# Kernel optimization log

Measured on AMD Instinct MI355X. Metric: run time of the kernel, lower is better.

The kernel has to match this reference:

```python
import jax, jax.numpy as jnp
import numpy as np

# Dimensions (TinyLlama-like)
B, T = 4, 1024
D = 2048          # hidden_size
H, DH = 32, 64    # heads, head_dim
HK = 8            # kv heads (GQA, n_rep = 4)
RQ, RKV = 32, 32  # per-head SVD ranks
RO, RF = 1024, 1024
I = 5632          # intermediate_size
THETA = 10000.0
EPS = 1e-5


def setup_inputs() -> dict:
    key = jax.random.key(0)
    ks = jax.random.split(key, 16)
    p = lambda k, s: jax.random.normal(k, s, jnp.float32) * 0.02
    return {
        "x": jax.random.normal(ks[0], (B, T, D), jnp.float32),
        "ln1_w": jnp.ones((D,), jnp.float32),
        "ln2_w": jnp.ones((D,), jnp.float32),
        "q_Us": p(ks[1], (H, DH, RQ)),  "q_V": p(ks[2], (H, RQ, D)),
        "k_Us": p(ks[3], (HK, DH, RKV)), "k_V": p(ks[4], (HK, RKV, D)),
        "v_Us": p(ks[5], (HK, DH, RKV)), "v_V": p(ks[6], (HK, RKV, D)),
        "o_Us": p(ks[7], (D, RO)),  "o_V": p(ks[8], (RO, H * DH)),
        "g_Us": p(ks[9], (I, RF)),  "g_V": p(ks[10], (RF, D)),
        "u_Us": p(ks[11], (I, RF)), "u_V": p(ks[12], (RF, D)),
        "d_Us": p(ks[13], (D, RF)), "d_V": p(ks[14], (RF, I)),
    }


def _rms(x, w):
    return x * jax.lax.rsqrt(jnp.mean(x * x, axis=-1, keepdims=True) + EPS) * w


def _rope_cos_sin(t_len, dh, dtype):
    half = dh // 2
    inv_freq = 1.0 / (THETA ** (jnp.arange(half, dtype=jnp.float32) / half))
    ang = jnp.arange(t_len, dtype=jnp.float32)[:, None] * inv_freq[None, :]  # [T, half]
    return jnp.cos(ang).astype(dtype), jnp.sin(ang).astype(dtype)


def _apply_rope(x, cos, sin):
    # x: [B,h,T,Dh], LLaMA half-split rotation
    half = x.shape[-1] // 2
    x1, x2 = x[..., :half], x[..., half:]
    c = cos[None, None]  # [1,1,T,half]
    s = sin[None, None]
    return jnp.concatenate([x1 * c - x2 * s, x2 * c + x1 * s], axis=-1)


def reference(x, ln1_w, ln2_w, q_Us, q_V, k_Us, k_V, v_Us, v_V,
              o_Us, o_V, g_Us, g_V, u_Us, u_V, d_Us, d_V):
    b, t, d = x.shape
    h1 = _rms(x, ln1_w)

    # per-head low-rank projections: y_h = x @ V_h^T @ Us_h^T
    q = jnp.einsum('bhtr,hdr->bhtd', jnp.einsum('btD,hrD->bhtr', h1, q_V), q_Us)  # [B,H,T,Dh]
    k = jnp.einsum('bhtr,hdr->bhtd', jnp.einsum('btD,hrD->bhtr', h1, k_V), k_Us)  # [B,Hk,T,Dh]
    v = jnp.einsum('bhtr,hdr->bhtd', jnp.einsum('btD,hrD->bhtr', h1, v_V), v_Us)

    cos, sin = _rope_cos_sin(t, DH, x.dtype)
    q = _apply_rope(q, cos, sin)
    k = _apply_rope(k, cos, sin)

    n_rep = H // HK
    k = jnp.repeat(k, n_rep, axis=1)  # _repeat_kv
    v = jnp.repeat(v, n_rep, axis=1)

    scale = 1.0 / np.sqrt(DH)
    scores = jnp.einsum('bhtd,bhsd->bhts', q, k) * scale
    causal = jnp.tril(jnp.ones((t, t), bool))
    scores = jnp.where(causal[None, None], scores, jnp.finfo(scores.dtype).min)
    attn = jax.nn.softmax(scores, axis=-1)
    ctx = jnp.einsum('bhts,bhsd->bhtd', attn, v)
    ctx = ctx.transpose(0, 2, 1, 3).reshape(b, t, H * DH)

    # low-rank output proj: o = ctx @ o_V^T @ o_Us^T
    attn_out = jnp.einsum('btr,Dr->btD', jnp.einsum('btk,rk->btr', ctx, o_V), o_Us)
    x = x + attn_out

    # SwiGLU MLP with low-rank factors
    h2 = _rms(x, ln2_w)
    g = jnp.einsum('btr,ir->bti', jnp.einsum('btD,rD->btr', h2, g_V), g_Us)
    u = jnp.einsum('btr,ir->bti', jnp.einsum('btD,rD->btr', h2, u_V), u_Us)
    ff = jax.nn.silu(g) * u
    down = jnp.einsum('btr,Dr->btD', jnp.einsum('bti,ri->btr', ff, d_V), d_Us)
    return x + down
```

## Files before the change

### kernel.cpp

```cpp
#include <hip/hip_runtime.h>
#include <math.h>

typedef unsigned short u16;
typedef unsigned int u32;
typedef __bf16 bf16x8 __attribute__((ext_vector_type(8)));
typedef float f32x4 __attribute__((ext_vector_type(4)));

__device__ __forceinline__ float bf2f(u16 u) {
  union { u32 i; float f; } x; x.i = ((u32)u) << 16; return x.f;
}
__device__ __forceinline__ u16 f2bf(float f) {
  union { float f; u32 i; } x; x.f = f;
  return (u16)((x.i + 0x7fffu + ((x.i >> 16) & 1u)) >> 16);
}

#define GLDS16(gp, lp)                                                        \
  __builtin_amdgcn_global_load_lds(                                           \
      (const __attribute__((address_space(1))) u32*)(gp),                     \
      (__attribute__((address_space(3))) u32*)(lp), 16, 0, 0)

__global__ void detect_k(const u16* __restrict__ w, int* __restrict__ flag) {
  if (threadIdx.x == 0 && blockIdx.x == 0)
    *flag = (w[0] == 0x0000u && w[1] == 0x3F80u) ? 1 : 0;
}

struct CvtArgs {
  const void* src[17];
  u32 dstOff[17];
  u32 blkOff[18];
};

__global__ __launch_bounds__(256) void cvt_all(CvtArgs a, u16* __restrict__ dstB,
                                               const int* __restrict__ flag) {
  int seg = 0;
  const int bx = blockIdx.x;
#pragma unroll 1
  while (bx >= (int)a.blkOff[seg + 1]) seg++;
  const long local = ((long)(bx - a.blkOff[seg]) * 256 + threadIdx.x) * 8;
  u16* dst = dstB + a.dstOff[seg] + local;
  if (*flag) {
    const float* s = (const float*)a.src[seg] + local;
    float4 va = *(const float4*)(s);
    float4 vb = *(const float4*)(s + 4);
    uint4 o; u16* op = (u16*)&o;
    op[0] = f2bf(va.x); op[1] = f2bf(va.y); op[2] = f2bf(va.z); op[3] = f2bf(va.w);
    op[4] = f2bf(vb.x); op[5] = f2bf(vb.y); op[6] = f2bf(vb.z); op[7] = f2bf(vb.w);
    *(uint4*)dst = o;
  } else {
    *(uint4*)dst = *(const uint4*)((const u16*)a.src[seg] + local);
  }
}

__global__ __launch_bounds__(256) void rms_k(const u16* __restrict__ x,
                                             const u16* __restrict__ w,
                                             u16* __restrict__ out) {
  const long row = blockIdx.x;
  const u16* xr = x + row * 2048;
  u16* orow = out + row * 2048;
  const int tid = threadIdx.x;
  const int base = tid * 8;
  uint4 u = *(const uint4*)(xr + base);
  const u16* us = (const u16*)&u;
  float v[8];
  float ss = 0.f;
#pragma unroll
  for (int i = 0; i < 8; i++) { v[i] = bf2f(us[i]); ss += v[i] * v[i]; }
#pragma unroll
  for (int off = 32; off > 0; off >>= 1) ss += __shfl_xor(ss, off);
  __shared__ float red[4];
  if ((tid & 63) == 0) red[tid >> 6] = ss;
  __syncthreads();
  float total = red[0] + red[1] + red[2] + red[3];
  float inv = rsqrtf(total * (1.0f / 2048.0f) + 1e-5f);
  uint4 wv = *(const uint4*)(w + base);
  const u16* wp = (const u16*)&wv;
  uint4 o;
  u16* op = (u16*)&o;
#pragma unroll
  for (int i = 0; i < 8; i++) op[i] = f2bf(v[i] * inv * bf2f(wp[i]));
  *(uint4*)(orow + base) = o;
}

template <int EPI>
__global__ __launch_bounds__(256, 2) void gemm_bt(const u16* __restrict__ A,
                                                  const u16* __restrict__ B,
                                                  void* Cv,
                                                  const u16* R,
                                                  const int* flagp,
                                                  int N, int Klen, int lda, int ldb) {
  __shared__ u16 As[128 * 32];
  __shared__ u16 Bs[128 * 32];
  const int m0 = blockIdx.y * 128;
  const int n0 = blockIdx.x * 128;
  const int tid = threadIdx.x;
  const int wave = tid >> 6;
  const int lane = tid & 63;
  const int wr = (wave >> 1) * 64;
  const int wc = (wave & 1) * 64;
  const int l16 = lane & 15;
  const int quad = lane >> 4;
  u16* C = (u16*)Cv;
  float* Cf = (float*)Cv;
  bool f32o = false;
  if (EPI == 3) f32o = (*flagp != 0);

  f32x4 acc[4][4];
#pragma unroll
  for (int i = 0; i < 4; i++)
#pragma unroll
    for (int j = 0; j < 4; j++) acc[i][j] = (f32x4){0.f, 0.f, 0.f, 0.f};

  const int srow = wave * 16 + (lane >> 2);
  const int scol = (lane & 3) * 8;
  const u16* Ag = A + (long)(m0 + srow) * lda + scol;
  const u16* Bg = B + (long)(n0 + srow) * ldb + scol;
  const long astep = (long)64 * lda;
  const long bstep = (long)64 * ldb;
  u16* Asw = &As[wave * 16 * 32];
  u16* Bsw = &Bs[wave * 16 * 32];

  for (int k0 = 0; k0 < Klen; k0 += 32) {
    GLDS16(Ag + k0, Asw);
    GLDS16(Ag + astep + k0, Asw + 64 * 32);
    GLDS16(Bg + k0, Bsw);
    GLDS16(Bg + bstep + k0, Bsw + 64 * 32);
    __syncthreads();
    bf16x8 af[4], bfr[4];
#pragma unroll
    for (int t = 0; t < 4; t++) {
      af[t]  = *(const bf16x8*)(&As[(wr + t * 16 + l16) * 32 + quad * 8]);
      bfr[t] = *(const bf16x8*)(&Bs[(wc + t * 16 + l16) * 32 + quad * 8]);
    }
#pragma unroll
    for (int i = 0; i < 4; i++)
#pragma unroll
      for (int j = 0; j < 4; j++)
        acc[i][j] = __builtin_amdgcn_mfma_f32_16x16x32_bf16(bfr[j], af[i], acc[i][j], 0, 0, 0);
    __syncthreads();
  }

#pragma unroll
  for (int i = 0; i < 4; i++) {
    const int m = m0 + wr + i * 16 + l16;
#pragma unroll
    for (int j = 0; j < 4; j++) {
      const int n = n0 + wc + j * 16 + quad * 4;
      const long idx = (long)m * N + n;
      float v[4];
#pragma unroll
      for (int r = 0; r < 4; r++) v[r] = acc[i][j][r];
      if (EPI == 1 || EPI == 3) {
        uint2 rr = *(const uint2*)(R + idx);
        const u16* rp = (const u16*)&rr;
#pragma unroll
        for (int r = 0; r < 4; r++) v[r] += bf2f(rp[r]);
      }
      if (EPI == 3 && f32o) {
        float4 o = {v[0], v[1], v[2], v[3]};
        *(float4*)(Cf + idx) = o;
      } else {
        uint2 o; u16* op = (u16*)&o;
#pragma unroll
        for (int r = 0; r < 4; r++) op[r] = f2bf(v[r]);
        *(uint2*)(C + idx) = o;
      }
    }
  }
}

__global__ __launch_bounds__(256, 2) void gemm_silu(const u16* __restrict__ Agp,
                                                    const u16* __restrict__ Aup,
                                                    const u16* __restrict__ Bgp,
                                                    const u16* __restrict__ Bup,
                                                    u16* __restrict__ C,
                                                    int N, int Klen, int lda, int ldb) {
  __shared__ u16 Asg[128 * 32];
  __shared__ u16 Asu[128 * 32];
  __shared__ u16 Bsg[128 * 32];
  __shared__ u16 Bsu[128 * 32];
  const int m0 = blockIdx.y * 128;
  const int n0 = blockIdx.x * 128;
  const int tid = threadIdx.x;
  const int wave = tid >> 6;
  const int lane = tid & 63;
  const int wr = (wave >> 1) * 64;
  const int wc = (wave & 1) * 64;
  const int l16 = lane & 15;
  const int quad = lane >> 4;

  f32x4 ag[4][4], au[4][4];
#pragma unroll
  for (int i = 0; i < 4; i++)
#pragma unroll
    for (int j = 0; j < 4; j++) {
      ag[i][j] = (f32x4){0.f, 0.f, 0.f, 0.f};
      au[i][j] = (f32x4){0.f, 0.f, 0.f, 0.f};
    }

  const int srow = wave * 16 + (lane >> 2);
  const int scol = (lane & 3) * 8;
  const u16* Ag_ = Agp + (long)(m0 + srow) * lda + scol;
  const u16* Au_ = Aup + (long)(m0 + srow) * lda + scol;
  const u16* Bg_ = Bgp + (long)(n0 + srow) * ldb + scol;
  const u16* Bu_ = Bup + (long)(n0 + srow) * ldb + scol;
  const long astep = (long)64 * lda;
  const long bstep = (long)64 * ldb;
  u16* Asgw = &Asg[wave * 16 * 32];
  u16* Asuw = &Asu[wave * 16 * 32];
  u16* Bsgw = &Bsg[wave * 16 * 32];
  u16* Bsuw = &Bsu[wave * 16 * 32];

  for (int k0 = 0; k0 < Klen; k0 += 32) {
    GLDS16(Ag_ + k0, Asgw);
    GLDS16(Ag_ + astep + k0, Asgw + 64 * 32);
    GLDS16(Au_ + k0, Asuw);
    GLDS16(Au_ + astep + k0, Asuw + 64 * 32);
    GLDS16(Bg_ + k0, Bsgw);
    GLDS16(Bg_ + bstep + k0, Bsgw + 64 * 32);
    GLDS16(Bu_ + k0, Bsuw);
    GLDS16(Bu_ + bstep + k0, Bsuw + 64 * 32);
    __syncthreads();
    bf16x8 afg[4], afu[4], bfg[4], bfu[4];
#pragma unroll
    for (int t = 0; t < 4; t++) {
      afg[t] = *(const bf16x8*)(&Asg[(wr + t * 16 + l16) * 32 + quad * 8]);
      afu[t] = *(const bf16x8*)(&Asu[(wr + t * 16 + l16) * 32 + quad * 8]);
      bfg[t] = *(const bf16x8*)(&Bsg[(wc + t * 16 + l16) * 32 + quad * 8]);
      bfu[t] = *(const bf16x8*)(&Bsu[(wc + t * 16 + l16) * 32 + quad * 8]);
    }
#pragma unroll
    for (int i = 0; i < 4; i++)
#pragma unroll
      for (int j = 0; j < 4; j++) {
        ag[i][j] = __builtin_amdgcn_mfma_f32_16x16x32_bf16(bfg[j], afg[i], ag[i][j], 0, 0, 0);
        au[i][j] = __builtin_amdgcn_mfma_f32_16x16x32_bf16(bfu[j], afu[i], au[i][j], 0, 0, 0);
      }
    __syncthreads();
  }

#pragma unroll
  for (int i = 0; i < 4; i++) {
    const int m = m0 + wr + i * 16 + l16;
#pragma unroll
    for (int j = 0; j < 4; j++) {
      const int n = n0 + wc + j * 16 + quad * 4;
      const long idx = (long)m * N + n;
      uint2 o; u16* op = (u16*)&o;
#pragma unroll
      for (int r = 0; r < 4; r++) {
        float g = ag[i][j][r];
        float v = au[i][j][r] * g / (1.f + __expf(-g));
        op[r] = f2bf(v);
      }
      *(uint2*)(C + idx) = o;
    }
  }
}

__global__ __launch_bounds__(256) void combine2(const u16* __restrict__ a,
                                                const u16* __restrict__ b,
                                                u16* __restrict__ o) {
  const long i = ((long)blockIdx.x * 256 + threadIdx.x) * 8;
  uint4 ua = *(const uint4*)(a + i);
  uint4 ub = *(const uint4*)(b + i);
  const u16* pa = (const u16*)&ua;
  const u16* pb = (const u16*)&ub;
  uint4 uo; u16* po = (u16*)&uo;
#pragma unroll
  for (int j = 0; j < 8; j++) po[j] = f2bf(bf2f(pa[j]) + bf2f(pb[j]));
  *(uint4*)(o + i) = uo;
}

__global__ __launch_bounds__(256) void expand_k(const u16* __restrict__ rbuf,
                                                int rstride,
                                                const u16* __restrict__ Us,
                                                u16* __restrict__ out,
                                                int nheads, int doRope) {
  const int tok = blockIdx.x;
  const int wave = threadIdx.x >> 6;
  const int d = threadIdx.x & 63;
  const int h = blockIdx.y * 4 + wave;
  const int b = tok >> 10;
  const int t = tok & 1023;
  const u16* up = Us + ((long)h * 64 + d) * 32;
  const u16* rp = rbuf + (long)tok * rstride + h * 32;
  float s = 0.f;
#pragma unroll
  for (int c = 0; c < 4; c++) {
    uint4 uu = *(const uint4*)(up + c * 8);
    uint4 rr = *(const uint4*)(rp + c * 8);
    const u16* u8p = (const u16*)&uu;
    const u16* r8p = (const u16*)&rr;
#pragma unroll
    for (int i = 0; i < 8; i++) s += bf2f(u8p[i]) * bf2f(r8p[i]);
  }
  if (doRope) {
    const int j = d & 31;
    float inv = powf(10000.0f, -(float)j * (1.0f / 32.0f));
    float ang = (float)t * inv;
    float sn, cs;
    sincosf(ang, &sn, &cs);
    float partner = __shfl_xor(s, 32);
    s = (d < 32) ? (s * cs - partner * sn) : (s * cs + partner * sn);
  }
  out[(((long)(b * nheads + h)) * 1024 + t) * 64 + d] = f2bf(s);
}

__global__ __launch_bounds__(256) void vT_k(const u16* __restrict__ vbuf,
                                            u16* __restrict__ vT) {
  __shared__ u16 tile[64][72];
  const int b = blockIdx.z, kh = blockIdx.y;
  const int t0 = blockIdx.x * 64;
  const int tid = threadIdx.x;
  const int r = tid >> 2;
  const int c = (tid & 3) * 16;
  const u16* src = vbuf + ((long)(b * 8 + kh) * 1024 + t0 + r) * 64 + c;
  *(uint4*)&tile[r][c] = *(const uint4*)src;
  *(uint4*)&tile[r][c + 8] = *(const uint4*)(src + 8);
  __syncthreads();
  u16 tmp[16];
#pragma unroll
  for (int i = 0; i < 16; i++) tmp[i] = tile[c + i][r];
  u16* dst = vT + ((long)(b * 8 + kh) * 64 + r) * 1024 + t0 + c;
  *(uint4*)dst = *(uint4*)&tmp[0];
  *(uint4*)(dst + 8) = *(uint4*)&tmp[8];
}

#define ATS 72

__global__ __launch_bounds__(256, 2) void attn_mfma(const u16* __restrict__ q,
                                                    const u16* __restrict__ k,
                                                    const u16* __restrict__ vT,
                                                    u16* __restrict__ ctx) {
  __shared__ u16 Ks[64 * ATS];
  __shared__ u16 Vts[64 * ATS];
  __shared__ u16 Plds[4][16 * ATS];
  const int bx = blockIdx.x;
  const int h = blockIdx.y;
  const int b = blockIdx.z;
  const int kh = h >> 2;
  const int qlo = bx * 64;
  const int qhi = (15 - bx) * 64;
  const int tid = threadIdx.x;
  const int wave = tid >> 6;
  const int lane = tid & 63;
  const int l16 = lane & 15;
  const int quad = lane >> 4;

  const u16* qb = q + ((long)(b * 32 + h) * 1024) * 64;
  const u16* kb = k + ((long)(b * 8 + kh) * 1024) * 64;
  const u16* vb = vT + ((long)(b * 8 + kh) * 64) * 1024;

  bf16x8 qfl[2], qfh[2];
  {
    const u16* qp = qb + (long)(qlo + wave * 16 + l16) * 64 + quad * 8;
    qfl[0] = *(const bf16x8*)(qp);
    qfl[1] = *(const bf16x8*)(qp + 32);
    qp = qb + (long)(qhi + wave * 16 + l16) * 64 + quad * 8;
    qfh[0] = *(const bf16x8*)(qp);
    qfh[1] = *(const bf16x8*)(qp + 32);
  }

  float ml[4], ll[4], mh[4], lh[4];
  f32x4 ol[4], oh[4];
#pragma unroll
  for (int r = 0; r < 4; r++) { ml[r] = -1e30f; ll[r] = 0.f; mh[r] = -1e30f; lh[r] = 0.f; }
#pragma unroll
  for (int j = 0; j < 4; j++) { ol[j] = (f32x4){0.f, 0.f, 0.f, 0.f}; oh[j] = ol[j]; }

  const int srow = tid >> 2;
  const int sc0 = (tid & 3) * 16;
  int s0 = 0;

  auto process = [&](const bf16x8* qf, float* m, float* l, f32x4* oacc, int qtb) {
    f32x4 s[4];
#pragma unroll
    for (int t = 0; t < 4; t++) {
      s[t] = (f32x4){0.f, 0.f, 0.f, 0.f};
      const u16* kr = &Ks[(t * 16 + l16) * ATS + quad * 8];
      bf16x8 b0 = *(const bf16x8*)(kr);
      bf16x8 b1 = *(const bf16x8*)(kr + 32);
      s[t] = __builtin_amdgcn_mfma_f32_16x16x32_bf16(qf[0], b0, s[t], 0, 0, 0);
      s[t] = __builtin_amdgcn_mfma_f32_16x16x32_bf16(qf[1], b1, s[t], 0, 0, 0);
    }
#pragma unroll
    for (int t = 0; t < 4; t++) s[t] *= 0.125f;
    if (s0 == qtb) {
#pragma unroll
      for (int t = 0; t < 4; t++)
#pragma unroll
        for (int r = 0; r < 4; r++)
          if (s0 + t * 16 + l16 > qtb + wave * 16 + quad * 4 + r) s[t][r] = -1e30f;
    }
    float p[4][4];
#pragma unroll
    for (int r = 0; r < 4; r++) {
      float mx = fmaxf(fmaxf(s[0][r], s[1][r]), fmaxf(s[2][r], s[3][r]));
#pragma unroll
      for (int off = 1; off < 16; off <<= 1) mx = fmaxf(mx, __shfl_xor(mx, off));
      const float mnew = fmaxf(m[r], mx);
      const float alpha = __expf(m[r] - mnew);
      float ps = 0.f;
#pragma unroll
      for (int t = 0; t < 4; t++) { p[t][r] = __expf(s[t][r] - mnew); ps += p[t][r]; }
#pragma unroll
      for (int off = 1; off < 16; off <<= 1) ps += __shfl_xor(ps, off);
      l[r] = l[r] * alpha + ps;
      m[r] = mnew;
#pragma unroll
      for (int j = 0; j < 4; j++) oacc[j][r] *= alpha;
    }
    u16* pw = &Plds[wave][0];
#pragma unroll
    for (int t = 0; t < 4; t++)
#pragma unroll
      for (int r = 0; r < 4; r++)
        pw[(quad * 4 + r) * ATS + t * 16 + l16] = f2bf(p[t][r]);
    bf16x8 pf0 = *(const bf16x8*)(&pw[l16 * ATS + quad * 8]);
    bf16x8 pf1 = *(const bf16x8*)(&pw[l16 * ATS + 32 + quad * 8]);
#pragma unroll
    for (int j = 0; j < 4; j++) {
      const u16* vr = &Vts[(j * 16 + l16) * ATS + quad * 8];
      bf16x8 v0 = *(const bf16x8*)(vr);
      bf16x8 v1 = *(const bf16x8*)(vr + 32);
      oacc[j] = __builtin_amdgcn_mfma_f32_16x16x32_bf16(pf0, v0, oacc[j], 0, 0, 0);
      oacc[j] = __builtin_amdgcn_mfma_f32_16x16x32_bf16(pf1, v1, oacc[j], 0, 0, 0);
    }
  };

  for (s0 = 0; s0 <= qhi; s0 += 64) {
    __syncthreads();
    {
      const u16* kp = kb + (long)(s0 + srow) * 64 + sc0;
      *(uint4*)&Ks[srow * ATS + sc0] = *(const uint4*)kp;
      *(uint4*)&Ks[srow * ATS + sc0 + 8] = *(const uint4*)(kp + 8);
      const u16* vp = vb + (long)srow * 1024 + s0 + sc0;
      *(uint4*)&Vts[srow * ATS + sc0] = *(const uint4*)vp;
      *(uint4*)&Vts[srow * ATS + sc0 + 8] = *(const uint4*)(vp + 8);
    }
    __syncthreads();
    process(qfh, mh, lh, oh, qhi);
    if (s0 <= qlo) process(qfl, ml, ll, ol, qlo);
  }

#pragma unroll
  for (int r = 0; r < 4; r++) {
    const int rowl = qlo + wave * 16 + quad * 4 + r;
    const int rowh = qhi + wave * 16 + quad * 4 + r;
    const float il = 1.f / ll[r];
    const float ih = 1.f / lh[r];
#pragma unroll
    for (int j = 0; j < 4; j++) {
      ctx[(((long)(b * 1024 + rowl)) * 32 + h) * 64 + j * 16 + l16] = f2bf(ol[j][r] * il);
      ctx[(((long)(b * 1024 + rowh)) * 32 + h) * 64 + j * 16 + l16] = f2bf(oh[j][r] * ih);
    }
  }
}

extern "C" void kernel_launch(void* const* d_in, const int* in_sizes, int n_in,
                              void* d_out, int out_size, void* d_ws, size_t ws_size,
                              hipStream_t stream) {
  char* ws = (char*)d_ws;
  u16* cb = (u16*)ws;
  u16* cx    = cb + 0;
  u16* cln1  = cb + 8388608;
  u16* cln2  = cb + 8390656;
  u16* cqUs  = cb + 8392704;
  u16* ckUs  = cb + 8458240;
  u16* cvUs  = cb + 8474624;
  u16* cqkvV = cb + 8491008;
  u16* coUs  = cb + 11636736;
  u16* coV   = cb + 13733888;
  u16* cguV  = cb + 15831040;
  u16* cgUs  = cb + 20025344;
  u16* cuUs  = cb + 25792512;
  u16* cdUs  = cb + 31559680;
  u16* cdV   = cb + 33656832;

  char* P = ws + 78848000;
  u16* h1    = (u16*)(P + 0);
  u16* qkvr  = (u16*)(P + 16777216);
  u16* qp0   = (u16*)(P + 33554432);
  u16* qp1   = (u16*)(P + 46137344);
  u16* qbuf  = (u16*)(P + 33554432);
  u16* kbuf  = (u16*)(P + 50331648);
  u16* vbuf  = (u16*)(P + 54525952);
  u16* ctx   = (u16*)(P + 58720256);
  u16* vbufT = (u16*)(P + 75497472);
  u16* orr   = (u16*)(P + 75497472);
  u16* xmid  = (u16*)(P + 83886080);
  u16* op0   = (u16*)(P + 0);
  u16* op1   = (u16*)(P + 8388608);
  u16* h2    = (u16*)(P + 0);
  u16* gur   = (u16*)(P + 16777216);
  u16* gbuf  = (u16*)(P + 33554432);
  u16* dp0   = (u16*)(P + 0);
  u16* dp1   = (u16*)(P + 8388608);
  u16* dr    = (u16*)(P + 16777216);
  int* flag  = (int*)(ws + 179511296);

  const dim3 blk(256);
  detect_k<<<1, 64, 0, stream>>>((const u16*)d_in[1], flag);

  CvtArgs ca;
  const u32 dOff[17] = {0u, 8388608u, 8390656u, 8392704u, 8491008u, 8458240u,
                        10588160u, 8474624u, 11112448u, 11636736u, 13733888u,
                        20025344u, 15831040u, 25792512u, 17928192u, 31559680u,
                        33656832u};
  const u32 nblk[17] = {4096u, 1u, 1u, 32u, 1024u, 8u, 256u, 8u, 256u, 1024u,
                        1024u, 2816u, 1024u, 2816u, 1024u, 1024u, 2816u};
  u32 cum = 0;
  for (int i = 0; i < 17; i++) {
    ca.src[i] = d_in[i];
    ca.dstOff[i] = dOff[i];
    ca.blkOff[i] = cum;
    cum += nblk[i];
  }
  ca.blkOff[17] = cum;
  cvt_all<<<cum, blk, 0, stream>>>(ca, cb, flag);

  rms_k<<<4096, blk, 0, stream>>>(cx, cln1, h1);
  gemm_bt<0><<<dim3(12, 32), blk, 0, stream>>>(h1, cqkvV, qp0, nullptr, nullptr, 1536, 1024, 2048, 2048);
  gemm_bt<0><<<dim3(12, 32), blk, 0, stream>>>(h1 + 1024, cqkvV + 1024, qp1, nullptr, nullptr, 1536, 1024, 2048, 2048);
  combine2<<<3072, blk, 0, stream>>>(qp0, qp1, qkvr);
  expand_k<<<dim3(4096, 8), blk, 0, stream>>>(qkvr, 1536, cqUs, qbuf, 32, 1);
  expand_k<<<dim3(4096, 2), blk, 0, stream>>>(qkvr + 1024, 1536, ckUs, kbuf, 8, 1);
  expand_k<<<dim3(4096, 2), blk, 0, stream>>>(qkvr + 1280, 1536, cvUs, vbuf, 8, 0);
  vT_k<<<dim3(16, 8, 4), blk, 0, stream>>>(vbuf, vbufT);
  attn_mfma<<<dim3(8, 32, 4), blk, 0, stream>>>(qbuf, kbuf, vbufT, ctx);
  gemm_bt<0><<<dim3(8, 32), blk, 0, stream>>>(ctx, coV, op0, nullptr, nullptr, 1024, 1024, 2048, 2048);
  gemm_bt<0><<<dim3(8, 32), blk, 0, stream>>>(ctx + 1024, coV + 1024, op1, nullptr, nullptr, 1024, 1024, 2048, 2048);
  combine2<<<2048, blk, 0, stream>>>(op0, op1, orr);
  gemm_bt<1><<<dim3(16, 32), blk, 0, stream>>>(orr, coUs, xmid, cx, nullptr, 2048, 1024, 1024, 1024);
  rms_k<<<4096, blk, 0, stream>>>(xmid, cln2, h2);
  gemm_bt<0><<<dim3(16, 32), blk, 0, stream>>>(h2, cguV, gur, nullptr, nullptr, 2048, 2048, 2048, 2048);
  gemm_silu<<<dim3(44, 32), blk, 0, stream>>>(gur, gur + 1024, cgUs, cuUs, gbuf, 5632, 1024, 2048, 1024);
  gemm_bt<0><<<dim3(8, 32), blk, 0, stream>>>(gbuf, cdV, dp0, nullptr, nullptr, 1024, 2816, 5632, 5632);
  gemm_bt<0><<<dim3(8, 32), blk, 0, stream>>>(gbuf + 2816, cdV + 2816, dp1, nullptr, nullptr, 1024, 2816, 5632, 5632);
  combine2<<<2048, blk, 0, stream>>>(dp0, dp1, dr);
  gemm_bt<3><<<dim3(16, 32), blk, 0, stream>>>(dr, cdUs, d_out, xmid, flag, 2048, 1024, 1024, 1024);
}
```

Before: 861.0 us.

## Double-buffer LDS in fused gate/up SiLU GEMM and swizzle LDS columns

Converts the gemm_silu kernel's single-buffered LDS staging into a two-stage pipeline, issuing global-to-LDS loads for the next K tile before computing on the current one, with explicit vmcnt waits and barriers in place of __syncthreads. It also XOR-swizzles the 16-byte column chunk both on the store side (global source column) and on the fragment read side, to reduce LDS bank conflicts. The goal is to hide global load latency and speed up LDS reads. In exchange, LDS use doubles to 64KB per block, which may limit the two-blocks-per-CU occupancy target, and the hand-written waitcnt values must match the number of outstanding loads.

```diff
diff --git a/kernel.cpp b/kernel.cpp
--- a/kernel.cpp
+++ b/kernel.cpp
@@ -168,16 +168,28 @@
   }
 }
 
+#define STAGE_SILU(buf, k0)                                                   \
+  do {                                                                        \
+    GLDS16(Ag_ + (k0), &Asg[buf][woff]);                                      \
+    GLDS16(Ag_ + astep + (k0), &Asg[buf][woff + 64 * 32]);                    \
+    GLDS16(Au_ + (k0), &Asu[buf][woff]);                                      \
+    GLDS16(Au_ + astep + (k0), &Asu[buf][woff + 64 * 32]);                    \
+    GLDS16(Bg_ + (k0), &Bsg[buf][woff]);                                      \
+    GLDS16(Bg_ + bstep + (k0), &Bsg[buf][woff + 64 * 32]);                    \
+    GLDS16(Bu_ + (k0), &Bsu[buf][woff]);                                      \
+    GLDS16(Bu_ + bstep + (k0), &Bsu[buf][woff + 64 * 32]);                    \
+  } while (0)
+
 __global__ __launch_bounds__(256, 2) void gemm_silu(const u16* __restrict__ Agp,
                                                     const u16* __restrict__ Aup,
                                                     const u16* __restrict__ Bgp,
                                                     const u16* __restrict__ Bup,
                                                     u16* __restrict__ C,
                                                     int N, int Klen, int lda, int ldb) {
-  __shared__ u16 Asg[128 * 32];
-  __shared__ u16 Asu[128 * 32];
-  __shared__ u16 Bsg[128 * 32];
-  __shared__ u16 Bsu[128 * 32];
+  __shared__ u16 Asg[2][128 * 32];
+  __shared__ u16 Asu[2][128 * 32];
+  __shared__ u16 Bsg[2][128 * 32];
+  __shared__ u16 Bsu[2][128 * 32];
   const int m0 = blockIdx.y * 128;
   const int n0 = blockIdx.x * 128;
   const int tid = threadIdx.x;
@@ -198,35 +210,34 @@
     }
 
   const int srow = wave * 16 + (lane >> 2);
-  const int scol = (lane & 3) * 8;
+  const int scol = ((lane & 3) ^ ((lane >> 3) & 3)) * 8;
   const u16* Ag_ = Agp + (long)(m0 + srow) * lda + scol;
   const u16* Au_ = Aup + (long)(m0 + srow) * lda + scol;
   const u16* Bg_ = Bgp + (long)(n0 + srow) * ldb + scol;
   const u16* Bu_ = Bup + (long)(n0 + srow) * ldb + scol;
   const long astep = (long)64 * lda;
   const long bstep = (long)64 * ldb;
-  u16* Asgw = &Asg[wave * 16 * 32];
-  u16* Asuw = &Asu[wave * 16 * 32];
-  u16* Bsgw = &Bsg[wave * 16 * 32];
-  u16* Bsuw = &Bsu[wave * 16 * 32];
-
-  for (int k0 = 0; k0 < Klen; k0 += 32) {
-    GLDS16(Ag_ + k0, Asgw);
-    GLDS16(Ag_ + astep + k0, Asgw + 64 * 32);
-    GLDS16(Au_ + k0, Asuw);
-    GLDS16(Au_ + astep + k0, Asuw + 64 * 32);
-    GLDS16(Bg_ + k0, Bsgw);
-    GLDS16(Bg_ + bstep + k0, Bsgw + 64 * 32);
-    GLDS16(Bu_ + k0, Bsuw);
-    GLDS16(Bu_ + bstep + k0, Bsuw + 64 * 32);
-    __syncthreads();
+  const int woff = wave * 16 * 32;
+  const int rsw = (quad ^ ((l16 >> 1) & 3)) * 8;
+
+  const int nk = Klen >> 5;
+  STAGE_SILU(0, 0);
+  int cur = 0;
+  for (int kt = 0; kt < nk; ++kt) {
+    if (kt + 1 < nk) {
+      STAGE_SILU(cur ^ 1, (kt + 1) << 5);
+      asm volatile("s_waitcnt vmcnt(8)" ::: "memory");
+    } else {
+      asm volatile("s_waitcnt vmcnt(0)" ::: "memory");
+    }
+    asm volatile("s_barrier" ::: "memory");
     bf16x8 afg[4], afu[4], bfg[4], bfu[4];
 #pragma unroll
     for (int t = 0; t < 4; t++) {
-      afg[t] = *(const bf16x8*)(&Asg[(wr + t * 16 + l16) * 32 + quad * 8]);
-      afu[t] = *(const bf16x8*)(&Asu[(wr + t * 16 + l16) * 32 + quad * 8]);
-      bfg[t] = *(const bf16x8*)(&Bsg[(wc + t * 16 + l16) * 32 + quad * 8]);
-      bfu[t] = *(const bf16x8*)(&Bsu[(wc + t * 16 + l16) * 32 + quad * 8]);
+      afg[t] = *(const bf16x8*)(&Asg[cur][(wr + t * 16 + l16) * 32 + rsw]);
+      afu[t] = *(const bf16x8*)(&Asu[cur][(wr + t * 16 + l16) * 32 + rsw]);
+      bfg[t] = *(const bf16x8*)(&Bsg[cur][(wc + t * 16 + l16) * 32 + rsw]);
+      bfu[t] = *(const bf16x8*)(&Bsu[cur][(wc + t * 16 + l16) * 32 + rsw]);
     }
 #pragma unroll
     for (int i = 0; i < 4; i++)
@@ -235,7 +246,8 @@
         ag[i][j] = __builtin_amdgcn_mfma_f32_16x16x32_bf16(bfg[j], afg[i], ag[i][j], 0, 0, 0);
         au[i][j] = __builtin_amdgcn_mfma_f32_16x16x32_bf16(bfu[j], afu[i], au[i][j], 0, 0, 0);
       }
-    __syncthreads();
+    asm volatile("s_barrier" ::: "memory");
+    cur ^= 1;
   }
 
 #pragma unroll
```

Result: no change. 854.5 us (-0.8%).
